# Optimization experiments

Measured on AMD Instinct MI355X. Metric: run time of the kernel, lower is better.

Reference implementation:

```python
import jax, jax.numpy as jnp
import numpy as np

N, E_DIM, T = 32, 512, 2048
N_E = 8192
BETA = 0.25

def setup_inputs() -> dict:
    key = jax.random.key(0)
    k1, k2 = jax.random.split(key)
    z = jax.random.normal(k1, (N, E_DIM, T), dtype=jnp.float32)
    # nn.Embedding weight initialized uniform(-1/n_e, 1/n_e)
    emb = jax.random.uniform(k2, (N_E, E_DIM), dtype=jnp.float32,
                             minval=-1.0 / N_E, maxval=1.0 / N_E)
    return {"z": z, "emb": emb}

def reference(z, emb):
    n, width, t = z.shape
    # preprocess: (N, C, T) -> (N, T, C) -> (N*T, C)
    zf = jnp.transpose(z, (0, 2, 1)).reshape(-1, width)  # [M, e_dim]
    # squared euclidean distances: ||z||^2 + ||e||^2 - 2 z e^T
    d = (jnp.sum(zf ** 2, axis=1, keepdims=True)
         + jnp.sum(emb ** 2, axis=1)
         - 2.0 * jnp.matmul(zf, emb.T))  # [M, n_e]
    idx = jnp.argmin(d, axis=1)  # [M]
    z_q = emb[idx]  # [M, e_dim]
    sg = jax.lax.stop_gradient
    loss = jnp.mean((z_q - sg(zf)) ** 2) + BETA * jnp.mean((sg(z_q) - zf) ** 2)
    # straight-through estimator
    z_q = zf + sg(z_q - zf)
    # (N*T, C) -> (N, T, C) -> (N, C, T)
    z_q = jnp.transpose(z_q.reshape(n, t, width), (0, 2, 1))
    # perplexity from codebook usage histogram
    one_hot = jax.nn.one_hot(idx, emb.shape[0], dtype=zf.dtype)  # [M, n_e]
    e_mean = jnp.mean(one_hot, axis=0)
    perplexity = jnp.exp(-jnp.sum(e_mean * jnp.log(e_mean + 1e-10)))
    return (z_q, loss, perplexity)
```

## Files before the change

kernel.cpp:

```cpp
#include <hip/hip_runtime.h>
#include <stdint.h>

#define NE 8192
#define KD 512
#define MT 65536

typedef __attribute__((ext_vector_type(8))) short bf16x8;
typedef __attribute__((ext_vector_type(4))) float f32x4;

union U128 { uint4 u; bf16x8 b; };

#define WS_SUMZ2   0
#define WS_SUMSMIN 4
#define WS_HIST    8
#define WS_ZEROSZ  40960
#define WS_E2      40960
#define WS_IDX     73728
#define WS_EMB16   335872
#define WS_Z16     8724480

__device__ __forceinline__ unsigned int f2bf(float f) {
    union { float f; unsigned int u; } c; c.f = f;
    return (c.u + 0x7FFFu + ((c.u >> 16) & 1u)) >> 16;
}

__device__ __forceinline__ void load_lds16(const void* g, void* l) {
    __builtin_amdgcn_global_load_lds((const __attribute__((address_space(1))) void*)g,
                                     (__attribute__((address_space(3))) void*)l,
                                     16, 0, 0);
}

__global__ void k_embprep(const float* __restrict__ emb,
                          unsigned short* __restrict__ emb16,
                          float* __restrict__ e2) {
    const int code = blockIdx.x;
    const int lane = threadIdx.x;
    const float4* row = (const float4*)(emb + (size_t)code * KD);
    float4 a = row[lane * 2];
    float4 b = row[lane * 2 + 1];
    float s = a.x*a.x + a.y*a.y + a.z*a.z + a.w*a.w
            + b.x*b.x + b.y*b.y + b.z*b.z + b.w*b.w;
    uint4 o;
    o.x = f2bf(a.x) | (f2bf(a.y) << 16);
    o.y = f2bf(a.z) | (f2bf(a.w) << 16);
    o.z = f2bf(b.x) | (f2bf(b.y) << 16);
    o.w = f2bf(b.z) | (f2bf(b.w) << 16);
    ((uint4*)(emb16 + (size_t)code * KD))[lane] = o;
    #pragma unroll
    for (int off = 32; off; off >>= 1) s += __shfl_down(s, off, 64);
    if (lane == 0) e2[code] = s;
}

__global__ void k_zprep(const float* __restrict__ z,
                        unsigned short* __restrict__ z16,
                        float* __restrict__ sumz2) {
    __shared__ float arr[64][65];
    __shared__ float red[4];
    const int tid = threadIdx.x;
    const int n  = blockIdx.z;
    const int c0 = blockIdx.y * 64;
    const int t0 = blockIdx.x * 64;
    const int tl = tid & 63;
    const int cw = tid >> 6;
    const float* base = z + ((size_t)n * KD + c0) * 2048 + t0;
    float s = 0.f;
    #pragma unroll
    for (int u = 0; u < 16; u++) {
        int c = u * 4 + cw;
        float v = base[(size_t)c * 2048 + tl];
        arr[c][tl] = v;
        s += v * v;
    }
    #pragma unroll
    for (int off = 32; off; off >>= 1) s += __shfl_down(s, off, 64);
    if (tl == 0) red[cw] = s;
    __syncthreads();
    if (tid == 0) atomicAdd(sumz2, red[0] + red[1] + red[2] + red[3]);
    #pragma unroll
    for (int iter = 0; iter < 2; iter++) {
        int task = iter * 256 + tid;
        int row = task >> 3;
        int ch  = task & 7;
        float f0 = arr[ch*8+0][row], f1 = arr[ch*8+1][row],
              f2v = arr[ch*8+2][row], f3 = arr[ch*8+3][row],
              f4 = arr[ch*8+4][row], f5 = arr[ch*8+5][row],
              f6 = arr[ch*8+6][row], f7 = arr[ch*8+7][row];
        uint4 o;
        o.x = f2bf(f0) | (f2bf(f1) << 16);
        o.y = f2bf(f2v) | (f2bf(f3) << 16);
        o.z = f2bf(f4) | (f2bf(f5) << 16);
        o.w = f2bf(f6) | (f2bf(f7) << 16);
        *(uint4*)(z16 + ((size_t)(n * 2048 + t0 + row)) * KD + c0 + ch * 8) = o;
    }
}

__global__ __launch_bounds__(512, 2) void k_main(
    const unsigned short* __restrict__ z16,
    const unsigned short* __restrict__ emb16,
    const float* __restrict__ e2,
    int* __restrict__ g_idx,
    int* __restrict__ hist,
    float* __restrict__ sums)
{
    __shared__ __align__(16) unsigned short zt[128 * 512];
    __shared__ __align__(16) unsigned short et[2][256 * 32];

    const int tid  = threadIdx.x;
    const int lane = tid & 63;
    const int w    = tid >> 6;
    const int wm   = w & 1;
    const int wn   = w >> 1;
    const int quad = lane >> 4;
    const int col  = lane & 15;
    const int m0   = blockIdx.x * 128;

    {
        const int r  = tid >> 2;
        const int jb = (tid & 3) << 4;
        const uint4* gz = (const uint4*)(z16 + (size_t)(m0 + r) * KD);
        uint4* zt4w = (uint4*)zt;
        #pragma unroll
        for (int jj = 0; jj < 16; jj++) {
            int j  = jb + jj;
            int js = (j & 56) | ((j ^ r) & 7);
            zt4w[r * 64 + js] = gz[j];
        }
    }

    const int st_nl0 = w * 16 + (lane >> 2);
    const int st_q   = ((lane & 3) - ((st_nl0 >> 1) & 3)) & 3;
    const int st_q8  = st_q * 8;
    unsigned short* st_l0 = &et[0][0] + w * 512 + lane * 8;
    unsigned short* st_l1 = &et[0][0] + 4096 + w * 512 + lane * 8;

    f32x4 acc[4][4];
    #pragma unroll
    for (int mf = 0; mf < 4; mf++)
        #pragma unroll
        for (int nf = 0; nf < 4; nf++)
            acc[mf][nf] = (f32x4){0.f, 0.f, 0.f, 0.f};

    float rbv[4][4]; int rbi[4][4];
    #pragma unroll
    for (int mf = 0; mf < 4; mf++)
        #pragma unroll
        for (int rg = 0; rg < 4; rg++) { rbv[mf][rg] = 3.0e38f; rbi[mf][rg] = 0; }

    int zbase[4], r7[4];
    #pragma unroll
    for (int mf = 0; mf < 4; mf++) {
        int r = wm * 64 + mf * 16 + col;
        zbase[mf] = r * 64;
        r7[mf] = r & 7;
    }
    int bidx[4];
    #pragma unroll
    for (int nf = 0; nf < 4; nf++) {
        int nn = wn * 64 + nf * 16 + col;
        bidx[nf] = nn * 4 + ((quad + (nn >> 1)) & 3);
    }

    const uint4* zt4 = (const uint4*)zt;
    const uint4* et4[2] = { (const uint4*)&et[0][0], (const uint4*)&et[1][0] };

    {
        const unsigned short* g0 = emb16 + ((size_t)(st_nl0) << 9) + st_q8;
        const unsigned short* g1 = emb16 + ((size_t)(128 + st_nl0) << 9) + st_q8;
        load_lds16(g0, st_l0);
        load_lds16(g1, st_l1);
    }

    #pragma unroll 1
    for (int chunk = 0; chunk < 32; chunk++) {
        #pragma unroll
        for (int kk = 0; kk < 16; kk++) {
            __syncthreads();
            const int nxt = chunk * 16 + kk + 1;
            if (nxt < 512) {
                const int nchunk = nxt >> 4, nkk = nxt & 15, nbuf = nxt & 1;
                const size_t koff = (size_t)nkk * 32 + st_q8;
                const unsigned short* g0 = emb16 + (((size_t)(nchunk * 256 + st_nl0)) << 9) + koff;
                const unsigned short* g1 = emb16 + (((size_t)(nchunk * 256 + 128 + st_nl0)) << 9) + koff;
                load_lds16(g0, st_l0 + nbuf * 8192);
                load_lds16(g1, st_l1 + nbuf * 8192);
            }
            const int buf = kk & 1;
            const int jhi  = (kk * 4) & 56;
            const int jlow = ((kk & 1) << 2) | quad;
            bf16x8 af[4], bfv[4];
            #pragma unroll
            for (int mf = 0; mf < 4; mf++) {
                U128 u; u.u = zt4[zbase[mf] + (jhi | (jlow ^ r7[mf]))];
                af[mf] = u.b;
            }
            #pragma unroll
            for (int nf = 0; nf < 4; nf++) {
                U128 u; u.u = et4[buf][bidx[nf]];
                bfv[nf] = u.b;
            }
            #pragma unroll
            for (int mf = 0; mf < 4; mf++)
                #pragma unroll
                for (int nf = 0; nf < 4; nf++)
                    acc[mf][nf] = __builtin_amdgcn_mfma_f32_16x16x32_bf16(
                        af[mf], bfv[nf], acc[mf][nf], 0, 0, 0);
        }
        const int nb = chunk * 256 + wn * 64 + col;
        float e2v[4];
        #pragma unroll
        for (int nf = 0; nf < 4; nf++) e2v[nf] = e2[nb + nf * 16];
        #pragma unroll
        for (int mf = 0; mf < 4; mf++) {
            #pragma unroll
            for (int rg = 0; rg < 4; rg++) {
                float v0 = fmaf(-2.f, acc[mf][0][rg], e2v[0]);
                float v1 = fmaf(-2.f, acc[mf][1][rg], e2v[1]);
                float v2 = fmaf(-2.f, acc[mf][2][rg], e2v[2]);
                float v3 = fmaf(-2.f, acc[mf][3][rg], e2v[3]);
                float bv = v0; int bn = 0;
                if (v1 < bv) { bv = v1; bn = 1; }
                if (v2 < bv) { bv = v2; bn = 2; }
                if (v3 < bv) { bv = v3; bn = 3; }
                if (bv < rbv[mf][rg]) { rbv[mf][rg] = bv; rbi[mf][rg] = nb + (bn << 4); }
            }
            #pragma unroll
            for (int nf = 0; nf < 4; nf++)
                acc[mf][nf] = (f32x4){0.f, 0.f, 0.f, 0.f};
        }
    }

    #pragma unroll
    for (int mf = 0; mf < 4; mf++) {
        #pragma unroll
        for (int rg = 0; rg < 4; rg++) {
            float bv = rbv[mf][rg]; int bi = rbi[mf][rg];
            #pragma unroll
            for (int off = 1; off < 16; off <<= 1) {
                float ov = __shfl_xor(bv, off, 64);
                int   oi = __shfl_xor(bi, off, 64);
                if (ov < bv || (ov == bv && oi < bi)) { bv = ov; bi = oi; }
            }
            rbv[mf][rg] = bv; rbi[mf][rg] = bi;
        }
    }

    __syncthreads();
    float* sv = (float*)&et[0][0];
    int*   si = (int*)(sv + 512);
    if (col == 0) {
        #pragma unroll
        for (int mf = 0; mf < 4; mf++)
            #pragma unroll
            for (int rg = 0; rg < 4; rg++) {
                int rl = wm * 64 + mf * 16 + quad * 4 + rg;
                sv[wn * 128 + rl] = rbv[mf][rg];
                si[wn * 128 + rl] = rbi[mf][rg];
            }
    }
    __syncthreads();
    float myv = 0.f;
    if (tid < 128) {
        float bv = sv[tid]; int bi = si[tid];
        #pragma unroll
        for (int wnn = 1; wnn < 4; wnn++) {
            float ov = sv[wnn * 128 + tid]; int oi = si[wnn * 128 + tid];
            if (ov < bv || (ov == bv && oi < bi)) { bv = ov; bi = oi; }
        }
        g_idx[m0 + tid] = bi;
        atomicAdd(&hist[bi], 1);
        myv = bv;
    }
    #pragma unroll
    for (int off = 32; off; off >>= 1) myv += __shfl_down(myv, off, 64);
    if (lane == 0 && w < 2) atomicAdd(&sums[1], myv);
}

__global__ void k_final(const int* __restrict__ hist,
                        const float* __restrict__ sums,
                        float* __restrict__ out_scalars) {
    __shared__ float red[4];
    const int tid = threadIdx.x;
    float s = 0.f;
    for (int i = tid; i < NE; i += 256) {
        float e = (float)hist[i] * (1.0f / 65536.0f);
        s += e * logf(e + 1e-10f);
    }
    #pragma unroll
    for (int off = 32; off; off >>= 1) s += __shfl_down(s, off, 64);
    if ((tid & 63) == 0) red[tid >> 6] = s;
    __syncthreads();
    if (tid == 0) {
        float total = red[0] + red[1] + red[2] + red[3];
        float perp = expf(-total);
        float loss = 1.25f * (sums[0] + sums[1]) / (65536.0f * 512.0f);
        out_scalars[0] = loss;
        out_scalars[1] = perp;
    }
}

__global__ void k_gather(const float* __restrict__ emb,
                         const int* __restrict__ idx,
                         float* __restrict__ out) {
    __shared__ int ids[256];
    const int n  = blockIdx.y;
    const int t0 = blockIdx.x * 256;
    const int tid = threadIdx.x;
    ids[tid] = idx[n * 2048 + t0 + tid];
    __syncthreads();
    const int tq = tid & 63;
    const int cg = tid >> 6;
    const float* e0 = emb + (size_t)ids[tq * 4 + 0] * KD;
    const float* e1 = emb + (size_t)ids[tq * 4 + 1] * KD;
    const float* e2p = emb + (size_t)ids[tq * 4 + 2] * KD;
    const float* e3 = emb + (size_t)ids[tq * 4 + 3] * KD;
    for (int cb = cg * 4; cb < KD; cb += 16) {
        float4 a = *(const float4*)(e0 + cb);
        float4 b = *(const float4*)(e1 + cb);
        float4 c = *(const float4*)(e2p + cb);
        float4 d = *(const float4*)(e3 + cb);
        float* op = out + ((size_t)(n * KD + cb)) * 2048 + t0 + tq * 4;
        float4 o0 = {a.x, b.x, c.x, d.x};
        float4 o1 = {a.y, b.y, c.y, d.y};
        float4 o2 = {a.z, b.z, c.z, d.z};
        float4 o3 = {a.w, b.w, c.w, d.w};
        *(float4*)(op)        = o0;
        *(float4*)(op + 2048) = o1;
        *(float4*)(op + 4096) = o2;
        *(float4*)(op + 6144) = o3;
    }
}

extern "C" void kernel_launch(void* const* d_in, const int* in_sizes, int n_in,
                              void* d_out, int out_size, void* d_ws, size_t ws_size,
                              hipStream_t stream) {
    (void)in_sizes; (void)n_in; (void)out_size; (void)ws_size;
    const float* z   = (const float*)d_in[0];
    const float* emb = (const float*)d_in[1];
    float* out = (float*)d_out;
    char* ws = (char*)d_ws;

    float*          sums  = (float*)(ws + WS_SUMZ2);
    int*            hist  = (int*)(ws + WS_HIST);
    float*          e2    = (float*)(ws + WS_E2);
    int*            g_idx = (int*)(ws + WS_IDX);
    unsigned short* emb16 = (unsigned short*)(ws + WS_EMB16);
    unsigned short* z16   = (unsigned short*)(ws + WS_Z16);

    hipMemsetAsync(ws, 0, WS_ZEROSZ, stream);

    k_embprep<<<NE, 64, 0, stream>>>(emb, emb16, e2);
    k_zprep<<<dim3(32, 8, 32), 256, 0, stream>>>(z, z16, sums);
    k_main<<<512, 512, 0, stream>>>(z16, emb16, e2, g_idx, hist, sums);
    k_final<<<1, 256, 0, stream>>>(hist, sums, out + 33554432);
    k_gather<<<dim3(8, 32), 256, 0, stream>>>(emb, g_idx, out);
}
```

Before: 918.5 us.

## Load codebook tiles directly into registers instead of LDS double-buffering

Drops the shared-memory double buffer for embedding tiles, which was filled with global_load_lds and guarded by a block-wide barrier at every k-step. Each wave now reads its B fragments straight from global memory into registers, prefetching two steps ahead, and the later reduction scratch reuses the z tile buffer. This removes hundreds of barriers per block and frees LDS. In exchange, waves that share the same codebook columns now load the same data twice, the per-lane 16-byte row-strided reads coalesce poorly, and a two-step prefetch may not hide global/L2 latency. The final prefetches also read past the end of the codebook buffer into adjacent workspace.

```diff
diff --git a/kernel.cpp b/kernel.cpp
--- a/kernel.cpp
+++ b/kernel.cpp
@@ -22,12 +22,6 @@
 __device__ __forceinline__ unsigned int f2bf(float f) {
     union { float f; unsigned int u; } c; c.f = f;
     return (c.u + 0x7FFFu + ((c.u >> 16) & 1u)) >> 16;
-}
-
-__device__ __forceinline__ void load_lds16(const void* g, void* l) {
-    __builtin_amdgcn_global_load_lds((const __attribute__((address_space(1))) void*)g,
-                                     (__attribute__((address_space(3))) void*)l,
-                                     16, 0, 0);
 }
 
 __global__ void k_embprep(const float* __restrict__ emb,
@@ -103,7 +97,6 @@
     float* __restrict__ sums)
 {
     __shared__ __align__(16) unsigned short zt[128 * 512];
-    __shared__ __align__(16) unsigned short et[2][256 * 32];
 
     const int tid  = threadIdx.x;
     const int lane = tid & 63;
@@ -126,12 +119,7 @@
             zt4w[r * 64 + js] = gz[j];
         }
     }
-
-    const int st_nl0 = w * 16 + (lane >> 2);
-    const int st_q   = ((lane & 3) - ((st_nl0 >> 1) & 3)) & 3;
-    const int st_q8  = st_q * 8;
-    unsigned short* st_l0 = &et[0][0] + w * 512 + lane * 8;
-    unsigned short* st_l1 = &et[0][0] + 4096 + w * 512 + lane * 8;
+    __syncthreads();
 
     f32x4 acc[4][4];
     #pragma unroll
@@ -153,62 +141,63 @@
         zbase[mf] = r * 64;
         r7[mf] = r & 7;
     }
-    int bidx[4];
-    #pragma unroll
-    for (int nf = 0; nf < 4; nf++) {
-        int nn = wn * 64 + nf * 16 + col;
-        bidx[nf] = nn * 4 + ((quad + (nn >> 1)) & 3);
-    }
+    int rboff[4];
+    #pragma unroll
+    for (int nf = 0; nf < 4; nf++)
+        rboff[nf] = (wn * 64 + nf * 16 + col) * KD + quad * 8;
 
     const uint4* zt4 = (const uint4*)zt;
-    const uint4* et4[2] = { (const uint4*)&et[0][0], (const uint4*)&et[1][0] };
-
-    {
-        const unsigned short* g0 = emb16 + ((size_t)(st_nl0) << 9) + st_q8;
-        const unsigned short* g1 = emb16 + ((size_t)(128 + st_nl0) << 9) + st_q8;
-        load_lds16(g0, st_l0);
-        load_lds16(g1, st_l1);
-    }
+
+    bf16x8 b0[4], b1[4];
+
+    auto loadB = [&](int g, bf16x8 (&dst)[4]) {
+        const unsigned short* p = emb16 + (((size_t)(unsigned)(g >> 4)) << 17)
+                                        + ((unsigned)(g & 15) << 5);
+        #pragma unroll
+        for (int nf = 0; nf < 4; nf++) {
+            U128 u; u.u = *(const uint4*)(p + rboff[nf]);
+            dst[nf] = u.b;
+        }
+    };
+
+    auto doStep = [&](int kk, int g, bf16x8 (&bbuf)[4]) {
+        const int jhi  = (kk * 4) & 56;
+        const int jlow = ((kk & 1) << 2) | quad;
+        bf16x8 af[4], bcur[4];
+        #pragma unroll
+        for (int mf = 0; mf < 4; mf++) {
+            U128 u; u.u = zt4[zbase[mf] + (jhi | (jlow ^ r7[mf]))];
+            af[mf] = u.b;
+        }
+        #pragma unroll
+        for (int nf = 0; nf < 4; nf++) bcur[nf] = bbuf[nf];
+        loadB(g + 2, bbuf);
+        #pragma unroll
+        for (int mf = 0; mf < 4; mf++)
+            #pragma unroll
+            for (int nf = 0; nf < 4; nf++)
+                acc[mf][nf] = __builtin_amdgcn_mfma_f32_16x16x32_bf16(
+                    af[mf], bcur[nf], acc[mf][nf], 0, 0, 0);
+    };
+
+    loadB(0, b0);
+    loadB(1, b1);
 
     #pragma unroll 1
     for (int chunk = 0; chunk < 32; chunk++) {
-        #pragma unroll
-        for (int kk = 0; kk < 16; kk++) {
-            __syncthreads();
-            const int nxt = chunk * 16 + kk + 1;
-            if (nxt < 512) {
-                const int nchunk = nxt >> 4, nkk = nxt & 15, nbuf = nxt & 1;
-                const size_t koff = (size_t)nkk * 32 + st_q8;
-                const unsigned short* g0 = emb16 + (((size_t)(nchunk * 256 + st_nl0)) << 9) + koff;
-                const unsigned short* g1 = emb16 + (((size_t)(nchunk * 256 + 128 + st_nl0)) << 9) + koff;
-                load_lds16(g0, st_l0 + nbuf * 8192);
-                load_lds16(g1, st_l1 + nbuf * 8192);
-            }
-            const int buf = kk & 1;
-            const int jhi  = (kk * 4) & 56;
-            const int jlow = ((kk & 1) << 2) | quad;
-            bf16x8 af[4], bfv[4];
-            #pragma unroll
-            for (int mf = 0; mf < 4; mf++) {
-                U128 u; u.u = zt4[zbase[mf] + (jhi | (jlow ^ r7[mf]))];
-                af[mf] = u.b;
-            }
-            #pragma unroll
-            for (int nf = 0; nf < 4; nf++) {
-                U128 u; u.u = et4[buf][bidx[nf]];
-                bfv[nf] = u.b;
-            }
-            #pragma unroll
-            for (int mf = 0; mf < 4; mf++)
-                #pragma unroll
-                for (int nf = 0; nf < 4; nf++)
-                    acc[mf][nf] = __builtin_amdgcn_mfma_f32_16x16x32_bf16(
-                        af[mf], bfv[nf], acc[mf][nf], 0, 0, 0);
-        }
         const int nb = chunk * 256 + wn * 64 + col;
         float e2v[4];
         #pragma unroll
         for (int nf = 0; nf < 4; nf++) e2v[nf] = e2[nb + nf * 16];
+
+        #pragma unroll 1
+        for (int kk2 = 0; kk2 < 8; kk2++) {
+            const int kk = kk2 * 2;
+            const int g  = chunk * 16 + kk;
+            doStep(kk,     g,     b0);
+            doStep(kk + 1, g + 1, b1);
+        }
+
         #pragma unroll
         for (int mf = 0; mf < 4; mf++) {
             #pragma unroll
@@ -245,7 +234,7 @@
     }
 
     __syncthreads();
-    float* sv = (float*)&et[0][0];
+    float* sv = (float*)zt;
     int*   si = (int*)(sv + 512);
     if (col == 0) {
         #pragma unroll
```

Measured after the change: 1.297 ms. +41.2%, slower.
